# Performance work log

Measured on AMD Instinct MI355X. Metric: run time of the kernel, lower is better.

Reference implementation:

```python
import jax, jax.numpy as jnp
import numpy as np

B, C, H, W = 4, 64, 256, 256
HEADS = 8
WIN = 8            # window_size = (8, 8)
SPA_INNER = 64


def setup_inputs() -> dict:
    key = jax.random.key(0)
    ks = jax.random.split(key, 13)
    r = lambda k, s: jax.random.normal(k, s, dtype=jnp.float32)
    lin = lambda k, out_d, in_d: r(k, (out_d, in_d)) * (1.0 / np.sqrt(in_d))
    seq = WIN * WIN
    return {
        "x": r(ks[0], (B, C, H, W)),
        "pan_feature": r(ks[1], (B, C // 2, H, W)),
        "W_pan_q": lin(ks[2], SPA_INNER // 2, C // 2),
        "W_pan_k": lin(ks[3], SPA_INNER // 2, C // 2),
        "W_v1": lin(ks[4], SPA_INNER, C),
        "W_v2": lin(ks[5], SPA_INNER, C),
        "W_k2": lin(ks[6], SPA_INNER // 2, C),
        "W_q1c": lin(ks[7], SPA_INNER // 2, C),
        "W_k1c": lin(ks[8], SPA_INNER // 2, C),
        "W_inner_out": lin(ks[9], C, SPA_INNER),
        "W_inter_out": lin(ks[10], C, SPA_INNER),
        # trunc_normal_(std=1, a=-2, b=2) learned positional biases
        "pos_inner": jnp.clip(r(ks[11], (1, HEADS, seq, seq)), -2.0, 2.0),
        "pos_color": jnp.clip(r(ks[12], (1, HEADS, SPA_INNER // 2, SPA_INNER // 2)), -2.0, 2.0),
    }


def _mha(q, k, v, pos, heads, scale):
    # q,k,v: [B', n, h*d]  -> standard MHA with additive positional bias
    Bp, n, _ = q.shape
    sp = lambda t: t.reshape(Bp, n, heads, -1).transpose(0, 2, 1, 3)  # b h n d
    qh, kh, vh = sp(q) * scale, sp(k), sp(v)
    attn = jax.nn.softmax(jnp.einsum('bhid,bhjd->bhij', qh, kh) + pos, axis=-1)
    o = jnp.einsum('bhij,bhjd->bhid', attn, vh)
    return o.transpose(0, 2, 1, 3).reshape(Bp, n, -1)


def _mha_color(q, k, v, pos, heads, scale):
    # torch rearranges 'b (h d) n -> b h n d': dim1 (window area) is split
    # into heads, attention runs over the channel axis (dim2).
    Bp, hd, n = q.shape
    sp = lambda t: t.reshape(Bp, heads, hd // heads, n).transpose(0, 1, 3, 2)  # b h n d
    qh, kh, vh = sp(q) * scale, sp(k), sp(v)
    attn = jax.nn.softmax(jnp.einsum('bhid,bhjd->bhij', qh, kh) + pos, axis=-1)
    o = jnp.einsum('bhij,bhjd->bhid', attn, vh)
    return o.transpose(0, 1, 3, 2).reshape(Bp, hd, n)


def _inter_attn(q, k, v, heads):
    # elementwise cosine-similarity gating over the head-dim, no softmax
    Bp, n, dq = q.shape
    qh = q.reshape(Bp, n, heads, dq // heads).transpose(0, 2, 3, 1)  # b h d n
    kh = k.reshape(Bp, n, heads, dq // heads).transpose(0, 2, 3, 1)
    vh = v.reshape(Bp, n, heads, -1).transpose(0, 2, 1, 3)           # b h n d
    cos = jnp.sum(qh * kh, axis=2) / (jnp.linalg.norm(qh, axis=2) * jnp.linalg.norm(kh, axis=2))  # b h n
    o = cos[..., None] * vh
    return o.transpose(0, 2, 1, 3).reshape(Bp, n, -1)


def reference(x, pan_feature, W_pan_q, W_pan_k, W_v1, W_v2, W_k2, W_q1c, W_k1c,
              W_inner_out, W_inter_out, pos_inner, pos_color):
    b, c, h, w = x.shape
    hl = wl = WIN
    hn, wn = h // hl, w // wl

    def part(t):  # b c (hn hl) (wn wl) -> (b hn wn) (hl wl) c
        bb, cc = t.shape[0], t.shape[1]
        return t.reshape(bb, cc, hn, hl, wn, wl).transpose(0, 2, 4, 3, 5, 1).reshape(bb * hn * wn, hl * wl, cc)

    pan = part(pan_feature)       # [B', 64, c//2]
    xf = part(x)                  # [B', 64, c]

    pan_q = pan @ W_pan_q.T       # [B', 64, spa_inner//2]
    pan_k = pan @ W_pan_k.T
    x_v1 = xf @ W_v1.T            # [B', 64, spa_inner]
    half = x_v1.shape[-1] // 2
    v1_pan, v1_color = x_v1[..., :half], x_v1[..., half:]

    # inner spatial attention (scale uses inner_dim=spa_inner_dim, as in source)
    scale_inner = (SPA_INNER // HEADS) ** -0.5
    out_pan = _mha(pan_q, pan_k, v1_pan, pos_inner, HEADS, scale_inner)

    # inner color attention (scale uses inner_dim=window area)
    q1c = xf @ W_q1c.T
    k1c = xf @ W_k1c.T
    scale_color = ((hl * wl) // HEADS) ** -0.5
    out_color = _mha_color(q1c, k1c, v1_color, pos_color, HEADS, scale_color)

    out = jnp.concatenate([out_pan, out_color], axis=-1) @ W_inner_out.T  # [B', 64, c]
    x_v2 = out @ W_v2.T
    x_k2 = out @ W_k2.T
    out = _inter_attn(pan_q, x_k2, x_v2, HEADS)
    out = out @ W_inter_out.T     # [B', 64, c]

    cc = out.shape[-1]
    # (b hn wn) (hl wl) c -> b c (hn hl) (wn wl)
    out = out.reshape(b, hn, wn, hl, wl, cc).transpose(0, 5, 1, 3, 2, 4).reshape(b, cc, h, w)
    return out
```

## Files before the change

### kernel.cpp

```cpp
#include <hip/hip_runtime.h>


typedef __attribute__((ext_vector_type(8))) short short8;
typedef __attribute__((ext_vector_type(4))) float floatx4;

#define CCH  64
#define HH   256
#define WWD  256
#define HWsz (HH*WWD)
#define CHW  (CCH*HH*WWD)

#define OWPQ  0
#define OWPK  1024
#define OWV1  2048
#define OWV2  6144
#define OWK2  10240
#define OWQ1C 12288
#define OWK1C 14336
#define OWIO  16384
#define OWINT 20480
#define WTOT  24576

__device__ __forceinline__ unsigned int f2bf_u(float f) {
    unsigned int u = __builtin_bit_cast(unsigned int, f);
    u += 0x7FFFu + ((u >> 16) & 1u);
    return u >> 16;
}
__device__ __forceinline__ float bfu2f(unsigned int b) {
    return __builtin_bit_cast(float, b << 16);
}

template <int K, int N, int SA, int SO>
__device__ __forceinline__ void proj(const float* __restrict__ A,
                                     const unsigned short* __restrict__ Wh,
                                     const unsigned short* __restrict__ Wl,
                                     float* __restrict__ O,
                                     int wave, int lane) {
    constexpr int KS = K / 32;
    constexpr int NT = N / 16;
    const int l15 = lane & 15;
    const int quad = lane >> 4;
    const int m0 = wave * 16;

    union Frag { short8 v; unsigned int u[4]; };
    Frag ah[KS], al[KS];
#pragma unroll
    for (int kk = 0; kk < KS; ++kk) {
        const float4* ap = (const float4*)(A + (m0 + l15) * SA + kk * 32 + quad * 8);
        float4 fa = ap[0], fb = ap[1];
        float ff[8] = {fa.x, fa.y, fa.z, fa.w, fb.x, fb.y, fb.z, fb.w};
#pragma unroll
        for (int j2 = 0; j2 < 4; ++j2) {
            float f0 = ff[2 * j2], f1 = ff[2 * j2 + 1];
            unsigned int h0 = f2bf_u(f0), h1 = f2bf_u(f1);
            float r0 = f0 - bfu2f(h0), r1 = f1 - bfu2f(h1);
            ah[kk].u[j2] = h0 | (h1 << 16);
            al[kk].u[j2] = f2bf_u(r0) | (f2bf_u(r1) << 16);
        }
    }

#pragma unroll
    for (int nt = 0; nt < NT; ++nt) {
        floatx4 acc = {0.f, 0.f, 0.f, 0.f};
#pragma unroll
        for (int kk = 0; kk < KS; ++kk) {
            const int wo = (nt * 16 + l15) * K + kk * 32 + quad * 8;
            short8 bh = *(const short8*)(Wh + wo);
            short8 bl = *(const short8*)(Wl + wo);
            acc = __builtin_amdgcn_mfma_f32_16x16x32_bf16(ah[kk].v, bh, acc, 0, 0, 0);
            acc = __builtin_amdgcn_mfma_f32_16x16x32_bf16(al[kk].v, bh, acc, 0, 0, 0);
            acc = __builtin_amdgcn_mfma_f32_16x16x32_bf16(ah[kk].v, bl, acc, 0, 0, 0);
        }
#pragma unroll
        for (int r = 0; r < 4; ++r)
            O[(m0 + quad * 4 + r) * SO + nt * 16 + l15] = acc[r];
    }
}

__global__ void cvt_w(const float* __restrict__ w0, const float* __restrict__ w1,
                      const float* __restrict__ w2, const float* __restrict__ w3,
                      const float* __restrict__ w4, const float* __restrict__ w5,
                      const float* __restrict__ w6, const float* __restrict__ w7,
                      const float* __restrict__ w8, unsigned short* __restrict__ o) {
    int i = blockIdx.x * 256 + threadIdx.x;
    const float* src; int off;
    if      (i < 1024)  { src = w0; off = 0; }
    else if (i < 2048)  { src = w1; off = 1024; }
    else if (i < 6144)  { src = w2; off = 2048; }
    else if (i < 10240) { src = w3; off = 6144; }
    else if (i < 12288) { src = w4; off = 10240; }
    else if (i < 14336) { src = w5; off = 12288; }
    else if (i < 16384) { src = w6; off = 14336; }
    else if (i < 20480) { src = w7; off = 16384; }
    else                { src = w8; off = 20480; }
    float f = src[i - off];
    unsigned int h = f2bf_u(f);
    o[i] = (unsigned short)h;
    o[WTOT + i] = (unsigned short)f2bf_u(f - bfu2f(h));
}

__global__ __launch_bounds__(256, 2) void in2ma_main(
    const float* __restrict__ x, const float* __restrict__ pan,
    const float* __restrict__ posi, const float* __restrict__ posc,
    const unsigned short* __restrict__ wb, float* __restrict__ out) {
    __shared__ __align__(16) float s_xf[64 * 68];
    __shared__ __align__(16) float s_cat[64 * 68];
    __shared__ __align__(16) float s_v1[64 * 66];
    __shared__ __align__(16) float s_qk[64 * 66];
    __shared__ __align__(16) float s_k2[64 * 34];

    const int tid  = threadIdx.x;
    const int wave = tid >> 6;
    const int lane = tid & 63;
    const int wid  = blockIdx.x;
    const int b    = wid >> 10;
    const int hn_i = (wid >> 5) & 31;
    const int wn_i = wid & 31;
    const int h0 = hn_i * 8, w0 = wn_i * 8;

    const float scale = 0.35355339059327373f;
    const unsigned short* wlo = wb + WTOT;

    {
        const int c = tid >> 2, i = tid & 3;
        const float* xp = x + (size_t)b * CHW + (size_t)c * HWsz + (size_t)h0 * WWD + w0;
#pragma unroll
        for (int r = 0; r < 2; ++r) {
            const int hl = i * 2 + r;
            const float4* p = (const float4*)(xp + hl * WWD);
            float4 a = p[0], q = p[1];
            float* d = s_xf + (hl * 8) * 68 + c;
            d[0 * 68] = a.x; d[1 * 68] = a.y; d[2 * 68] = a.z; d[3 * 68] = a.w;
            d[4 * 68] = q.x; d[5 * 68] = q.y; d[6 * 68] = q.z; d[7 * 68] = q.w;
        }
        if (tid < 128) {
            const int c2 = tid >> 2, i2 = tid & 3;
            const float* pp = pan + (size_t)b * (CHW / 2) + (size_t)c2 * HWsz + (size_t)h0 * WWD + w0;
#pragma unroll
            for (int r = 0; r < 2; ++r) {
                const int hl = i2 * 2 + r;
                const float4* p = (const float4*)(pp + hl * WWD);
                float4 a = p[0], q = p[1];
                float* d = s_cat + (hl * 8) * 68 + c2;
                d[0 * 68] = a.x; d[1 * 68] = a.y; d[2 * 68] = a.z; d[3 * 68] = a.w;
                d[4 * 68] = q.x; d[5 * 68] = q.y; d[6 * 68] = q.z; d[7 * 68] = q.w;
            }
        }
    }
    __syncthreads();

    proj<32, 32, 68, 66>(s_cat,      wb + OWPQ,  wlo + OWPQ,  s_qk,      wave, lane);
    proj<32, 32, 68, 66>(s_cat,      wb + OWPK,  wlo + OWPK,  s_qk + 32, wave, lane);
    proj<64, 64, 68, 66>(s_xf,       wb + OWV1,  wlo + OWV1,  s_v1,      wave, lane);
    proj<64, 32, 68, 68>(s_xf,       wb + OWQ1C, wlo + OWQ1C, s_cat + 32, wave, lane);
    proj<64, 32, 68, 34>(s_xf,       wb + OWK1C, wlo + OWK1C, s_k2,      wave, lane);
    __syncthreads();

#pragma unroll
    for (int hh = 0; hh < 2; ++hh) {
        const int h = wave + hh * 4;
        const float* qp = s_qk + lane * 66 + 4 * h;
        float q0 = qp[0], q1 = qp[1], q2 = qp[2], q3 = qp[3];
        const float4* pp4 = (const float4*)(posi + h * 4096 + lane * 64);
        float lrow[64];
        float s = 0.f;
#pragma unroll
        for (int t4 = 0; t4 < 16; ++t4) {
            float4 pv = pp4[t4];
            float pvv[4] = {pv.x, pv.y, pv.z, pv.w};
#pragma unroll
            for (int u = 0; u < 4; ++u) {
                const int t = t4 * 4 + u;
                const float* kp = s_qk + t * 66 + 32 + 4 * h;
                float d = q0 * kp[0] + q1 * kp[1] + q2 * kp[2] + q3 * kp[3];
                float e = __expf(d * scale + pvv[u]);
                lrow[t] = e; s += e;
            }
        }
        const float inv = 1.f / s;
        float o0 = 0.f, o1 = 0.f, o2 = 0.f, o3 = 0.f;
#pragma unroll
        for (int t = 0; t < 64; ++t) {
            const float* vp = s_v1 + t * 66 + 4 * h;
            float p = lrow[t];
            o0 += p * vp[0]; o1 += p * vp[1]; o2 += p * vp[2]; o3 += p * vp[3];
        }
        float* op = s_cat + lane * 68 + 4 * h;
        op[0] = o0 * inv; op[1] = o1 * inv; op[2] = o2 * inv; op[3] = o3 * inv;
    }

    {
        const int h = wave * 2 + (lane >> 5);
        const int i = lane & 31;
        float q[8];
#pragma unroll
        for (int j = 0; j < 8; ++j) q[j] = s_cat[(8 * h + j) * 68 + 32 + i];
        float lr[32];
#pragma unroll
        for (int j = 0; j < 8; ++j) {
            const float* kp = s_k2 + (8 * h + j) * 34;
            const float qj = q[j];
#pragma unroll
            for (int t = 0; t < 32; ++t) {
                float kv = kp[t];
                if (j == 0) lr[t] = qj * kv; else lr[t] += qj * kv;
            }
        }
        const float4* pp4 = (const float4*)(posc + h * 1024 + i * 32);
        float s = 0.f;
#pragma unroll
        for (int t4 = 0; t4 < 8; ++t4) {
            float4 pv = pp4[t4];
            float pvv[4] = {pv.x, pv.y, pv.z, pv.w};
#pragma unroll
            for (int u = 0; u < 4; ++u) {
                const int t = t4 * 4 + u;
                float e = __expf(lr[t] * scale + pvv[u]);
                lr[t] = e; s += e;
            }
        }
        const float inv = 1.f / s;
#pragma unroll
        for (int j = 0; j < 8; ++j) {
            const float* vp = s_v1 + (8 * h + j) * 66 + 32;
            float acc = 0.f;
#pragma unroll
            for (int t = 0; t < 32; ++t) acc += lr[t] * vp[t];
            s_cat[(8 * h + j) * 68 + 32 + i] = acc * inv;
        }
    }
    __syncthreads();

    proj<64, 64, 68, 68>(s_cat, wb + OWIO, wlo + OWIO, s_xf, wave, lane);
    proj<64, 64, 68, 66>(s_xf,  wb + OWV2, wlo + OWV2, s_v1, wave, lane);
    proj<64, 32, 68, 34>(s_xf,  wb + OWK2, wlo + OWK2, s_k2, wave, lane);
    __syncthreads();

    {
        const int t = tid & 63;
        const int hb = tid >> 6;
#pragma unroll
        for (int r = 0; r < 2; ++r) {
            const int h = hb + r * 4;
            const float* qp = s_qk + t * 66 + 4 * h;
            const float* kp = s_k2 + t * 34 + 4 * h;
            float q0 = qp[0], q1 = qp[1], q2 = qp[2], q3 = qp[3];
            float k0 = kp[0], k1 = kp[1], k2 = kp[2], k3 = kp[3];
            float qq = q0 * q0 + q1 * q1 + q2 * q2 + q3 * q3;
            float kk = k0 * k0 + k1 * k1 + k2 * k2 + k3 * k3;
            float qk = q0 * k0 + q1 * k1 + q2 * k2 + q3 * k3;
            float cosv = qk * rsqrtf(qq * kk);
            const float* vp = s_v1 + t * 66 + 8 * h;
            float* op = s_cat + t * 68 + 8 * h;
#pragma unroll
            for (int j = 0; j < 8; ++j) op[j] = cosv * vp[j];
        }
    }
    __syncthreads();

    proj<64, 64, 68, 66>(s_cat, wb + OWINT, wlo + OWINT, s_v1, wave, lane);
    __syncthreads();

    {
        const int c = tid >> 2, i = tid & 3;
        float* op = out + (size_t)b * CHW + (size_t)c * HWsz + (size_t)h0 * WWD + w0;
#pragma unroll
        for (int r = 0; r < 2; ++r) {
            const int hl = i * 2 + r;
            float v[8];
#pragma unroll
            for (int wl = 0; wl < 8; ++wl)
                v[wl] = s_v1[(hl * 8 + wl) * 66 + c];
            float4* q = (float4*)(op + hl * WWD);
            float4 q0; q0.x = v[0]; q0.y = v[1]; q0.z = v[2]; q0.w = v[3];
            float4 q1; q1.x = v[4]; q1.y = v[5]; q1.z = v[6]; q1.w = v[7];
            q[0] = q0; q[1] = q1;
        }
    }
}

extern "C" void kernel_launch(void* const* d_in, const int* in_sizes, int n_in,
                              void* d_out, int out_size, void* d_ws, size_t ws_size,
                              hipStream_t stream) {
    (void)in_sizes; (void)n_in; (void)out_size; (void)ws_size;
    const float* x    = (const float*)d_in[0];
    const float* pan  = (const float*)d_in[1];
    const float* posi = (const float*)d_in[11];
    const float* posc = (const float*)d_in[12];
    unsigned short* wb = (unsigned short*)d_ws;

    cvt_w<<<WTOT / 256, 256, 0, stream>>>(
        (const float*)d_in[2], (const float*)d_in[3], (const float*)d_in[4],
        (const float*)d_in[5], (const float*)d_in[6], (const float*)d_in[7],
        (const float*)d_in[8], (const float*)d_in[9], (const float*)d_in[10], wb);

    in2ma_main<<<4096, 256, 0, stream>>>(x, pan, posi, posc, wb, (float*)d_out);
}
```

Measured before the change: 464.9 us.

## Switch projections to single-pass fp16 MFMA with fp16 shared-memory activations

Replaces the three-pass split-bf16 (hi/lo) MFMA emulation of fp32 GEMMs with a single fp16 MFMA pass, and stores all intermediate activations in shared memory as fp16 instead of fp32. This cuts the MFMA count by a factor of three, removes the per-fragment split conversion, and halves LDS footprint, which allows raising launch bounds to 3 blocks per CU. The spatial attention loop is also fused so P·V accumulates online without a 64-entry register row. The cost is reduced precision: fp16 intermediates and weights may exceed tolerance for some inputs.

```diff
diff --git a/kernel.cpp b/kernel.cpp
--- a/kernel.cpp
+++ b/kernel.cpp
@@ -1,7 +1,8 @@
 #include <hip/hip_runtime.h>
 
 
-typedef __attribute__((ext_vector_type(8))) short short8;
+typedef _Float16 h8_t __attribute__((ext_vector_type(8)));
+typedef _Float16 h4_t __attribute__((ext_vector_type(4)));
 typedef __attribute__((ext_vector_type(4))) float floatx4;
 
 #define CCH  64
@@ -21,20 +22,10 @@
 #define OWINT 20480
 #define WTOT  24576
 
-__device__ __forceinline__ unsigned int f2bf_u(float f) {
-    unsigned int u = __builtin_bit_cast(unsigned int, f);
-    u += 0x7FFFu + ((u >> 16) & 1u);
-    return u >> 16;
-}
-__device__ __forceinline__ float bfu2f(unsigned int b) {
-    return __builtin_bit_cast(float, b << 16);
-}
-
 template <int K, int N, int SA, int SO>
-__device__ __forceinline__ void proj(const float* __restrict__ A,
-                                     const unsigned short* __restrict__ Wh,
-                                     const unsigned short* __restrict__ Wl,
-                                     float* __restrict__ O,
+__device__ __forceinline__ void proj(const _Float16* __restrict__ A,
+                                     const _Float16* __restrict__ W,
+                                     _Float16* __restrict__ O,
                                      int wave, int lane) {
     constexpr int KS = K / 32;
     constexpr int NT = N / 16;
@@ -42,38 +33,22 @@
     const int quad = lane >> 4;
     const int m0 = wave * 16;
 
-    union Frag { short8 v; unsigned int u[4]; };
-    Frag ah[KS], al[KS];
-#pragma unroll
-    for (int kk = 0; kk < KS; ++kk) {
-        const float4* ap = (const float4*)(A + (m0 + l15) * SA + kk * 32 + quad * 8);
-        float4 fa = ap[0], fb = ap[1];
-        float ff[8] = {fa.x, fa.y, fa.z, fa.w, fb.x, fb.y, fb.z, fb.w};
-#pragma unroll
-        for (int j2 = 0; j2 < 4; ++j2) {
-            float f0 = ff[2 * j2], f1 = ff[2 * j2 + 1];
-            unsigned int h0 = f2bf_u(f0), h1 = f2bf_u(f1);
-            float r0 = f0 - bfu2f(h0), r1 = f1 - bfu2f(h1);
-            ah[kk].u[j2] = h0 | (h1 << 16);
-            al[kk].u[j2] = f2bf_u(r0) | (f2bf_u(r1) << 16);
-        }
-    }
+    h8_t af[KS];
+#pragma unroll
+    for (int kk = 0; kk < KS; ++kk)
+        af[kk] = *(const h8_t*)(A + (m0 + l15) * SA + kk * 32 + quad * 8);
 
 #pragma unroll
     for (int nt = 0; nt < NT; ++nt) {
         floatx4 acc = {0.f, 0.f, 0.f, 0.f};
 #pragma unroll
         for (int kk = 0; kk < KS; ++kk) {
-            const int wo = (nt * 16 + l15) * K + kk * 32 + quad * 8;
-            short8 bh = *(const short8*)(Wh + wo);
-            short8 bl = *(const short8*)(Wl + wo);
-            acc = __builtin_amdgcn_mfma_f32_16x16x32_bf16(ah[kk].v, bh, acc, 0, 0, 0);
-            acc = __builtin_amdgcn_mfma_f32_16x16x32_bf16(al[kk].v, bh, acc, 0, 0, 0);
-            acc = __builtin_amdgcn_mfma_f32_16x16x32_bf16(ah[kk].v, bl, acc, 0, 0, 0);
+            h8_t bf = *(const h8_t*)(W + (nt * 16 + l15) * K + kk * 32 + quad * 8);
+            acc = __builtin_amdgcn_mfma_f32_16x16x32_f16(af[kk], bf, acc, 0, 0, 0);
         }
 #pragma unroll
         for (int r = 0; r < 4; ++r)
-            O[(m0 + quad * 4 + r) * SO + nt * 16 + l15] = acc[r];
+            O[(m0 + quad * 4 + r) * SO + nt * 16 + l15] = (_Float16)acc[r];
     }
 }
 
@@ -81,7 +56,7 @@
                       const float* __restrict__ w2, const float* __restrict__ w3,
                       const float* __restrict__ w4, const float* __restrict__ w5,
                       const float* __restrict__ w6, const float* __restrict__ w7,
-                      const float* __restrict__ w8, unsigned short* __restrict__ o) {
+                      const float* __restrict__ w8, _Float16* __restrict__ o) {
     int i = blockIdx.x * 256 + threadIdx.x;
     const float* src; int off;
     if      (i < 1024)  { src = w0; off = 0; }
@@ -93,21 +68,19 @@
     else if (i < 16384) { src = w6; off = 14336; }
     else if (i < 20480) { src = w7; off = 16384; }
     else                { src = w8; off = 20480; }
-    float f = src[i - off];
-    unsigned int h = f2bf_u(f);
-    o[i] = (unsigned short)h;
-    o[WTOT + i] = (unsigned short)f2bf_u(f - bfu2f(h));
-}
-
-__global__ __launch_bounds__(256, 2) void in2ma_main(
+    o[i] = (_Float16)src[i - off];
+}
+
+__global__ __launch_bounds__(256, 3) void in2ma_main(
     const float* __restrict__ x, const float* __restrict__ pan,
     const float* __restrict__ posi, const float* __restrict__ posc,
-    const unsigned short* __restrict__ wb, float* __restrict__ out) {
-    __shared__ __align__(16) float s_xf[64 * 68];
-    __shared__ __align__(16) float s_cat[64 * 68];
-    __shared__ __align__(16) float s_v1[64 * 66];
-    __shared__ __align__(16) float s_qk[64 * 66];
-    __shared__ __align__(16) float s_k2[64 * 34];
+    const _Float16* __restrict__ wb, float* __restrict__ out) {
+    __shared__ __align__(16) _Float16 s_xf[64 * 72];
+    __shared__ __align__(16) _Float16 s_cat[64 * 72];
+    __shared__ __align__(16) _Float16 s_v1[64 * 72];
+    __shared__ __align__(16) _Float16 s_pq[64 * 40];
+    __shared__ __align__(16) _Float16 s_pk[64 * 40];
+    __shared__ __align__(16) _Float16 s_k2[64 * 40];
 
     const int tid  = threadIdx.x;
     const int wave = tid >> 6;
@@ -119,7 +92,6 @@
     const int h0 = hn_i * 8, w0 = wn_i * 8;
 
     const float scale = 0.35355339059327373f;
-    const unsigned short* wlo = wb + WTOT;
 
     {
         const int c = tid >> 2, i = tid & 3;
@@ -129,9 +101,11 @@
             const int hl = i * 2 + r;
             const float4* p = (const float4*)(xp + hl * WWD);
             float4 a = p[0], q = p[1];
-            float* d = s_xf + (hl * 8) * 68 + c;
-            d[0 * 68] = a.x; d[1 * 68] = a.y; d[2 * 68] = a.z; d[3 * 68] = a.w;
-            d[4 * 68] = q.x; d[5 * 68] = q.y; d[6 * 68] = q.z; d[7 * 68] = q.w;
+            _Float16* d = s_xf + (hl * 8) * 72 + c;
+            d[0 * 72] = (_Float16)a.x; d[1 * 72] = (_Float16)a.y;
+            d[2 * 72] = (_Float16)a.z; d[3 * 72] = (_Float16)a.w;
+            d[4 * 72] = (_Float16)q.x; d[5 * 72] = (_Float16)q.y;
+            d[6 * 72] = (_Float16)q.z; d[7 * 72] = (_Float16)q.w;
         }
         if (tid < 128) {
             const int c2 = tid >> 2, i2 = tid & 3;
@@ -141,29 +115,31 @@
                 const int hl = i2 * 2 + r;
                 const float4* p = (const float4*)(pp + hl * WWD);
                 float4 a = p[0], q = p[1];
-                float* d = s_cat + (hl * 8) * 68 + c2;
-                d[0 * 68] = a.x; d[1 * 68] = a.y; d[2 * 68] = a.z; d[3 * 68] = a.w;
-                d[4 * 68] = q.x; d[5 * 68] = q.y; d[6 * 68] = q.z; d[7 * 68] = q.w;
-            }
-        }
-    }
-    __syncthreads();
-
-    proj<32, 32, 68, 66>(s_cat,      wb + OWPQ,  wlo + OWPQ,  s_qk,      wave, lane);
-    proj<32, 32, 68, 66>(s_cat,      wb + OWPK,  wlo + OWPK,  s_qk + 32, wave, lane);
-    proj<64, 64, 68, 66>(s_xf,       wb + OWV1,  wlo + OWV1,  s_v1,      wave, lane);
-    proj<64, 32, 68, 68>(s_xf,       wb + OWQ1C, wlo + OWQ1C, s_cat + 32, wave, lane);
-    proj<64, 32, 68, 34>(s_xf,       wb + OWK1C, wlo + OWK1C, s_k2,      wave, lane);
+                _Float16* d = s_cat + (hl * 8) * 72 + c2;
+                d[0 * 72] = (_Float16)a.x; d[1 * 72] = (_Float16)a.y;
+                d[2 * 72] = (_Float16)a.z; d[3 * 72] = (_Float16)a.w;
+                d[4 * 72] = (_Float16)q.x; d[5 * 72] = (_Float16)q.y;
+                d[6 * 72] = (_Float16)q.z; d[7 * 72] = (_Float16)q.w;
+            }
+        }
+    }
+    __syncthreads();
+
+    proj<32, 32, 72, 40>(s_cat, wb + OWPQ,  s_pq,       wave, lane);
+    proj<32, 32, 72, 40>(s_cat, wb + OWPK,  s_pk,       wave, lane);
+    proj<64, 64, 72, 72>(s_xf,  wb + OWV1,  s_v1,       wave, lane);
+    proj<64, 32, 72, 72>(s_xf,  wb + OWQ1C, s_cat + 32, wave, lane);
+    proj<64, 32, 72, 40>(s_xf,  wb + OWK1C, s_k2,       wave, lane);
     __syncthreads();
 
 #pragma unroll
     for (int hh = 0; hh < 2; ++hh) {
         const int h = wave + hh * 4;
-        const float* qp = s_qk + lane * 66 + 4 * h;
-        float q0 = qp[0], q1 = qp[1], q2 = qp[2], q3 = qp[3];
+        h4_t q4 = *(const h4_t*)(s_pq + lane * 40 + 4 * h);
+        const float q0 = (float)q4.x, q1 = (float)q4.y,
+                    q2 = (float)q4.z, q3 = (float)q4.w;
         const float4* pp4 = (const float4*)(posi + h * 4096 + lane * 64);
-        float lrow[64];
-        float s = 0.f;
+        float s = 0.f, o0 = 0.f, o1 = 0.f, o2 = 0.f, o3 = 0.f;
 #pragma unroll
         for (int t4 = 0; t4 < 16; ++t4) {
             float4 pv = pp4[t4];
@@ -171,22 +147,20 @@
 #pragma unroll
             for (int u = 0; u < 4; ++u) {
                 const int t = t4 * 4 + u;
-                const float* kp = s_qk + t * 66 + 32 + 4 * h;
-                float d = q0 * kp[0] + q1 * kp[1] + q2 * kp[2] + q3 * kp[3];
+                h4_t kv = *(const h4_t*)(s_pk + t * 40 + 4 * h);
+                h4_t vv = *(const h4_t*)(s_v1 + t * 72 + 4 * h);
+                float d = q0 * (float)kv.x + q1 * (float)kv.y +
+                          q2 * (float)kv.z + q3 * (float)kv.w;
                 float e = __expf(d * scale + pvv[u]);
-                lrow[t] = e; s += e;
+                s += e;
+                o0 += e * (float)vv.x; o1 += e * (float)vv.y;
+                o2 += e * (float)vv.z; o3 += e * (float)vv.w;
             }
         }
         const float inv = 1.f / s;
-        float o0 = 0.f, o1 = 0.f, o2 = 0.f, o3 = 0.f;
-#pragma unroll
-        for (int t = 0; t < 64; ++t) {
-            const float* vp = s_v1 + t * 66 + 4 * h;
-            float p = lrow[t];
-            o0 += p * vp[0]; o1 += p * vp[1]; o2 += p * vp[2]; o3 += p * vp[3];
-        }
-        float* op = s_cat + lane * 68 + 4 * h;
-        op[0] = o0 * inv; op[1] = o1 * inv; op[2] = o2 * inv; op[3] = o3 * inv;
+        h4_t ov; ov.x = (_Float16)(o0 * inv); ov.y = (_Float16)(o1 * inv);
+        ov.z = (_Float16)(o2 * inv); ov.w = (_Float16)(o3 * inv);
+        *(h4_t*)(s_cat + lane * 72 + 4 * h) = ov;
     }
 
     {
@@ -194,16 +168,22 @@
         const int i = lane & 31;
         float q[8];
 #pragma unroll
-        for (int j = 0; j < 8; ++j) q[j] = s_cat[(8 * h + j) * 68 + 32 + i];
+        for (int j = 0; j < 8; ++j) q[j] = (float)s_cat[(8 * h + j) * 72 + 32 + i];
         float lr[32];
 #pragma unroll
         for (int j = 0; j < 8; ++j) {
-            const float* kp = s_k2 + (8 * h + j) * 34;
+            const _Float16* kp = s_k2 + (8 * h + j) * 40;
             const float qj = q[j];
 #pragma unroll
-            for (int t = 0; t < 32; ++t) {
-                float kv = kp[t];
-                if (j == 0) lr[t] = qj * kv; else lr[t] += qj * kv;
+            for (int t4 = 0; t4 < 8; ++t4) {
+                h4_t kv = *(const h4_t*)(kp + 4 * t4);
+                if (j == 0) {
+                    lr[4 * t4] = qj * (float)kv.x; lr[4 * t4 + 1] = qj * (float)kv.y;
+                    lr[4 * t4 + 2] = qj * (float)kv.z; lr[4 * t4 + 3] = qj * (float)kv.w;
+                } else {
+                    lr[4 * t4] += qj * (float)kv.x; lr[4 * t4 + 1] += qj * (float)kv.y;
+                    lr[4 * t4 + 2] += qj * (float)kv.z; lr[4 * t4 + 3] += qj * (float)kv.w;
+                }
             }
         }
         const float4* pp4 = (const float4*)(posc + h * 1024 + i * 32);
@@ -222,18 +202,22 @@
         const float inv = 1.f / s;
 #pragma unroll
         for (int j = 0; j < 8; ++j) {
-            const float* vp = s_v1 + (8 * h + j) * 66 + 32;
+            const _Float16* vp = s_v1 + (8 * h + j) * 72 + 32;
             float acc = 0.f;
 #pragma unroll
-            for (int t = 0; t < 32; ++t) acc += lr[t] * vp[t];
-            s_cat[(8 * h + j) * 68 + 32 + i] = acc * inv;
-        }
-    }
-    __syncthreads();
-
-    proj<64, 64, 68, 68>(s_cat, wb + OWIO, wlo + OWIO, s_xf, wave, lane);
-    proj<64, 64, 68, 66>(s_xf,  wb + OWV2, wlo + OWV2, s_v1, wave, lane);
-    proj<64, 32, 68, 34>(s_xf,  wb + OWK2, wlo + OWK2, s_k2, wave, lane);
+            for (int t4 = 0; t4 < 8; ++t4) {
+                h4_t vv = *(const h4_t*)(vp + 4 * t4);
+                acc += lr[4 * t4] * (float)vv.x + lr[4 * t4 + 1] * (float)vv.y +
+                       lr[4 * t4 + 2] * (float)vv.z + lr[4 * t4 + 3] * (float)vv.w;
+            }
+            s_cat[(8 * h + j) * 72 + 32 + i] = (_Float16)(acc * inv);
+        }
+    }
+    __syncthreads();
+
+    proj<64, 64, 72, 72>(s_cat, wb + OWIO, s_xf, wave, lane);
+    proj<64, 64, 72, 72>(s_xf,  wb + OWV2, s_v1, wave, lane);
+    proj<64, 32, 72, 40>(s_xf,  wb + OWK2, s_k2, wave, lane);
     __syncthreads();
 
     {
@@ -242,23 +226,24 @@
 #pragma unroll
         for (int r = 0; r < 2; ++r) {
             const int h = hb + r * 4;
-            const float* qp = s_qk + t * 66 + 4 * h;
-            const float* kp = s_k2 + t * 34 + 4 * h;
-            float q0 = qp[0], q1 = qp[1], q2 = qp[2], q3 = qp[3];
-            float k0 = kp[0], k1 = kp[1], k2 = kp[2], k3 = kp[3];
+            h4_t qv = *(const h4_t*)(s_pq + t * 40 + 4 * h);
+            h4_t kv = *(const h4_t*)(s_k2 + t * 40 + 4 * h);
+            float q0 = (float)qv.x, q1 = (float)qv.y, q2 = (float)qv.z, q3 = (float)qv.w;
+            float k0 = (float)kv.x, k1 = (float)kv.y, k2 = (float)kv.z, k3 = (float)kv.w;
             float qq = q0 * q0 + q1 * q1 + q2 * q2 + q3 * q3;
             float kk = k0 * k0 + k1 * k1 + k2 * k2 + k3 * k3;
             float qk = q0 * k0 + q1 * k1 + q2 * k2 + q3 * k3;
             float cosv = qk * rsqrtf(qq * kk);
-            const float* vp = s_v1 + t * 66 + 8 * h;
-            float* op = s_cat + t * 68 + 8 * h;
-#pragma unroll
-            for (int j = 0; j < 8; ++j) op[j] = cosv * vp[j];
-        }
-    }
-    __syncthreads();
-
-    proj<64, 64, 68, 66>(s_cat, wb + OWINT, wlo + OWINT, s_v1, wave, lane);
+            h8_t vv = *(const h8_t*)(s_v1 + t * 72 + 8 * h);
+            h8_t ov;
+#pragma unroll
+            for (int j = 0; j < 8; ++j) ov[j] = (_Float16)(cosv * (float)vv[j]);
+            *(h8_t*)(s_cat + t * 72 + 8 * h) = ov;
+        }
+    }
+    __syncthreads();
+
+    proj<64, 64, 72, 72>(s_cat, wb + OWINT, s_v1, wave, lane);
     __syncthreads();
 
     {
@@ -270,7 +255,7 @@
             float v[8];
 #pragma unroll
             for (int wl = 0; wl < 8; ++wl)
-                v[wl] = s_v1[(hl * 8 + wl) * 66 + c];
+                v[wl] = (float)s_v1[(hl * 8 + wl) * 72 + c];
             float4* q = (float4*)(op + hl * WWD);
             float4 q0; q0.x = v[0]; q0.y = v[1]; q0.z = v[2]; q0.w = v[3];
             float4 q1; q1.x = v[4]; q1.y = v[5]; q1.z = v[6]; q1.w = v[7];
@@ -287,7 +272,7 @@
     const float* pan  = (const float*)d_in[1];
     const float* posi = (const float*)d_in[11];
     const float* posc = (const float*)d_in[12];
-    unsigned short* wb = (unsigned short*)d_ws;
+    _Float16* wb = (_Float16*)d_ws;
 
     cvt_w<<<WTOT / 256, 256, 0, stream>>>(
         (const float*)d_in[2], (const float*)d_in[3], (const float*)d_in[4],
```

Result: slower. 1.018 ms (+119.1%).
